# Kernel tuning notes

Hardware: AMD Instinct MI355X
Metric: run time of the kernel (lower is better)

## Reference

```python
import jax, jax.numpy as jnp
import numpy as np

N = 50000      # nodes
E = 800000     # edges (avg degree 16)
D_IN = 128
D_H = 256
NUM_LAYERS = 5


def setup_inputs() -> dict:
    key = jax.random.key(0)
    ks = jax.random.split(key, 12)
    s_in = 1.0 / np.sqrt(D_IN)
    s_h = 1.0 / np.sqrt(D_H)
    x = jax.random.normal(ks[0], (N, D_IN), jnp.float32)
    edge_index = jax.random.randint(ks[1], (2, E), 0, N, jnp.int32)
    eps_all = jnp.zeros((NUM_LAYERS,), jnp.float32)
    # torch Linear layout: weight [out, in], y = x @ W.T + b; scaled for stability
    w0_l0 = jax.random.normal(ks[2], (D_H, D_IN), jnp.float32) * s_in
    b0_l0 = jax.random.normal(ks[3], (D_H,), jnp.float32) * 0.01
    w1_l0 = jax.random.normal(ks[4], (D_H, D_H), jnp.float32) * s_h
    b1_l0 = jax.random.normal(ks[5], (D_H,), jnp.float32) * 0.01
    w0_rest = jax.random.normal(ks[6], (4, D_H, D_H), jnp.float32) * s_h
    b0_rest = jax.random.normal(ks[7], (4, D_H), jnp.float32) * 0.01
    w1_rest = jax.random.normal(ks[8], (4, D_H, D_H), jnp.float32) * s_h
    b1_rest = jax.random.normal(ks[9], (4, D_H), jnp.float32) * 0.01
    return {"x": x, "edge_index": edge_index, "eps_all": eps_all,
            "w0_l0": w0_l0, "b0_l0": b0_l0, "w1_l0": w1_l0, "b1_l0": b1_l0,
            "w0_rest": w0_rest, "b0_rest": b0_rest, "w1_rest": w1_rest, "b1_rest": b1_rest}


def _gin_layer(x, src, dst, eps, w0, b0, w1, b1):
    # gather source-node features along edges, scatter-sum into destination nodes
    aggr = jax.ops.segment_sum(x[src], dst, num_segments=N)  # [N, d]
    h = (1.0 + eps) * x + aggr
    h = jax.nn.relu(h @ w0.T + b0)   # dropout p=0.0 -> identity
    h = h @ w1.T + b1
    return jax.nn.relu(h)            # inter-layer ReLU from the trace


def reference(x, edge_index, eps_all, w0_l0, b0_l0, w1_l0, b1_l0,
              w0_rest, b0_rest, w1_rest, b1_rest):
    src = edge_index[0]  # edge_index_j (messages come from row 0)
    dst = edge_index[1]  # edge_index_i (aggregated at row 1)
    h = _gin_layer(x, src, dst, eps_all[0], w0_l0, b0_l0, w1_l0, b1_l0)
    for i in range(4):  # layers 1..4, identical shapes
        h = _gin_layer(h, src, dst, eps_all[i + 1],
                       w0_rest[i], b0_rest[i], w1_rest[i], b1_rest[i])
    return h  # [N, D_H]
```

## Files before the change

kernel.cpp:

```cpp
#include <hip/hip_runtime.h>
#include <hip/hip_bf16.h>
#include <stdint.h>

#define D_IN 128
#define D_H 256
#define NLAYERS 5

typedef __bf16 bf16x8 __attribute__((ext_vector_type(8)));
typedef float f32x4 __attribute__((ext_vector_type(4)));
typedef unsigned short u16x8 __attribute__((ext_vector_type(8)));

#define MID_STRIDE 260

__device__ inline unsigned short bfbits(float f) {
  __hip_bfloat16 h = __float2bfloat16(f);
  unsigned short s;
  __builtin_memcpy(&s, &h, 2);
  return s;
}

__device__ inline unsigned packbf(float lo, float hi) {
  return (unsigned)bfbits(lo) | ((unsigned)bfbits(hi) << 16);
}

__device__ inline void addbf2(float& a, float& b, unsigned u) {
  a += __uint_as_float(u << 16);
  b += __uint_as_float(u & 0xffff0000u);
}

__device__ inline void addbf2s(float& a, float& b, unsigned u, float s) {
  a += s * __uint_as_float(u << 16);
  b += s * __uint_as_float(u & 0xffff0000u);
}

__global__ void conv_inputs(const float* __restrict__ x, const float* __restrict__ a,
                            const float* __restrict__ b, const float* __restrict__ c,
                            const float* __restrict__ d,
                            __hip_bfloat16* __restrict__ xb,
                            __hip_bfloat16* __restrict__ wb, int nx) {
  int gid = blockIdx.x * blockDim.x + threadIdx.x;
  if (gid < nx) {
    xb[gid] = __float2bfloat16(x[gid]);
    return;
  }
  gid -= nx;
  if (gid >= 622592) return;
  float v;
  if (gid < 32768) v = a[gid];
  else if (gid < 98304) v = b[gid - 32768];
  else if (gid < 360448) v = c[gid - 98304];
  else v = d[gid - 360448];
  wb[gid] = __float2bfloat16(v);
}

__global__ void zero_ints(int* __restrict__ p, int n) {
  int i = blockIdx.x * blockDim.x + threadIdx.x;
  if (i < n) p[i] = 0;
}

#define CSR_CHUNKS 128

__global__ __launch_bounds__(256) void hist_kernel(const int* __restrict__ ei, int E,
                                                   int* __restrict__ deg, int N) {
  const int r = blockIdx.x & 7;
  const int chunk = blockIdx.x >> 3;
  const int rsize = (N + 7) >> 3;
  const int lo = r * rsize;
  const int hi = (lo + rsize < N) ? lo + rsize : N;
  const int stride = CSR_CHUNKS * 256;
  for (int e = chunk * 256 + threadIdx.x; e < E; e += stride) {
    int d = ei[E + e];
    if (d >= lo && d < hi) atomicAdd(&deg[d], 1);
  }
}

__global__ __launch_bounds__(256) void fill_kernel(const int* __restrict__ ei, int E,
                                                   const int* __restrict__ row_start,
                                                   int* __restrict__ cursor,
                                                   int* __restrict__ csr, int N) {
  const int r = blockIdx.x & 7;
  const int chunk = blockIdx.x >> 3;
  const int rsize = (N + 7) >> 3;
  const int lo = r * rsize;
  const int hi = (lo + rsize < N) ? lo + rsize : N;
  const int stride = CSR_CHUNKS * 256;
  for (int e = chunk * 256 + threadIdx.x; e < E; e += stride) {
    int d = ei[E + e];
    if (d >= lo && d < hi) {
      int p = atomicAdd(&cursor[d], 1);
      csr[row_start[d] + p] = ei[e];
    }
  }
}

__global__ __launch_bounds__(256) void block_sums(const int* __restrict__ deg,
                                                  int* __restrict__ bsum, int N) {
  int t = threadIdx.x;
  int idx = blockIdx.x * 1024 + t * 4;
  int4 v = {0, 0, 0, 0};
  if (idx + 3 < N) v = *reinterpret_cast<const int4*>(deg + idx);
  else {
    if (idx + 0 < N) v.x = deg[idx + 0];
    if (idx + 1 < N) v.y = deg[idx + 1];
    if (idx + 2 < N) v.z = deg[idx + 2];
    if (idx + 3 < N) v.w = deg[idx + 3];
  }
  int s = v.x + v.y + v.z + v.w;
#pragma unroll
  for (int off = 32; off > 0; off >>= 1) s += __shfl_down(s, off);
  __shared__ int ws[4];
  int lane = t & 63, w = t >> 6;
  if (lane == 0) ws[w] = s;
  __syncthreads();
  if (t == 0) bsum[blockIdx.x] = ws[0] + ws[1] + ws[2] + ws[3];
}

__global__ void scan_bsums(int* __restrict__ bsum, int nb) {
  int t = threadIdx.x;
  int orig = (t < nb) ? bsum[t] : 0;
  int v = orig;
#pragma unroll
  for (int off = 1; off < 64; off <<= 1) {
    int u = __shfl_up(v, off);
    if (t >= off) v += u;
  }
  if (t < nb) bsum[t] = v - orig;
}

__global__ __launch_bounds__(256) void scan_apply(const int* __restrict__ deg,
                                                  const int* __restrict__ bsum_ex,
                                                  int* __restrict__ row_start, int N) {
  int t = threadIdx.x;
  int idx = blockIdx.x * 1024 + t * 4;
  int4 v = {0, 0, 0, 0};
  if (idx + 3 < N) v = *reinterpret_cast<const int4*>(deg + idx);
  else {
    if (idx + 0 < N) v.x = deg[idx + 0];
    if (idx + 1 < N) v.y = deg[idx + 1];
    if (idx + 2 < N) v.z = deg[idx + 2];
    if (idx + 3 < N) v.w = deg[idx + 3];
  }
  int s = v.x + v.y + v.z + v.w;
  int lane = t & 63, w = t >> 6;
  int sc = s;
#pragma unroll
  for (int off = 1; off < 64; off <<= 1) {
    int u = __shfl_up(sc, off);
    if (lane >= off) sc += u;
  }
  __shared__ int woff[4];
  if (lane == 63) woff[w] = sc;
  __syncthreads();
  int boff = bsum_ex[blockIdx.x];
#pragma unroll
  for (int i = 0; i < 4; ++i)
    if (i < w) boff += woff[i];
  int ex = boff + sc - s;
  if (idx + 3 < N) {
    int4 o;
    o.x = ex;
    o.y = ex + v.x;
    o.z = ex + v.x + v.y;
    o.w = ex + v.x + v.y + v.z;
    *reinterpret_cast<int4*>(row_start + idx) = o;
  } else {
    if (idx + 0 < N) row_start[idx + 0] = ex;
    if (idx + 1 < N) row_start[idx + 1] = ex + v.x;
    if (idx + 2 < N) row_start[idx + 2] = ex + v.x + v.y;
    if (idx + 3 < N) row_start[idx + 3] = ex + v.x + v.y + v.z;
  }
}

template <int D>
__global__ __launch_bounds__(256) void aggregate(const unsigned short* __restrict__ hb,
                                                 const int* __restrict__ csr,
                                                 const int* __restrict__ row_start,
                                                 const int* __restrict__ deg,
                                                 const float* __restrict__ eps_all,
                                                 int layer,
                                                 unsigned short* __restrict__ pre,
                                                 int N) {
  constexpr int PL = D / 32;
  const int half = threadIdx.x >> 5;
  const int lane = threadIdx.x & 31;
  const int node = blockIdx.x * 8 + half;
  if (node >= N) return;

  const int start = row_start[node];
  const int cnt = deg[node];
  const float epsv = 1.0f + eps_all[layer];

  float acc[PL];
#pragma unroll
  for (int j = 0; j < PL; ++j) acc[j] = 0.0f;

  if (D == 256) {
    uint4 su = *reinterpret_cast<const uint4*>(hb + (size_t)node * D + lane * 8);
    for (int base = 0; base < cnt; base += 32) {
      int m = cnt - base;
      if (m > 32) m = 32;
      int idx = (lane < m) ? csr[start + base + lane] : 0;
      int i = 0;
      for (; i + 8 <= m; i += 8) {
        uint4 q[8];
#pragma unroll
        for (int r = 0; r < 8; ++r) {
          int s = __shfl(idx, i + r, 32);
          q[r] = *reinterpret_cast<const uint4*>(hb + (size_t)s * D + lane * 8);
        }
#pragma unroll
        for (int r = 0; r < 8; ++r) {
          addbf2(acc[0], acc[1], q[r].x);
          addbf2(acc[2], acc[3], q[r].y);
          addbf2(acc[4], acc[5], q[r].z);
          addbf2(acc[6], acc[7], q[r].w);
        }
      }
      for (; i + 4 <= m; i += 4) {
        uint4 q[4];
#pragma unroll
        for (int r = 0; r < 4; ++r) {
          int s = __shfl(idx, i + r, 32);
          q[r] = *reinterpret_cast<const uint4*>(hb + (size_t)s * D + lane * 8);
        }
#pragma unroll
        for (int r = 0; r < 4; ++r) {
          addbf2(acc[0], acc[1], q[r].x);
          addbf2(acc[2], acc[3], q[r].y);
          addbf2(acc[4], acc[5], q[r].z);
          addbf2(acc[6], acc[7], q[r].w);
        }
      }
      for (; i < m; ++i) {
        int s = __shfl(idx, i, 32);
        uint4 q = *reinterpret_cast<const uint4*>(hb + (size_t)s * D + lane * 8);
        addbf2(acc[0], acc[1], q.x);
        addbf2(acc[2], acc[3], q.y);
        addbf2(acc[4], acc[5], q.z);
        addbf2(acc[6], acc[7], q.w);
      }
    }
    addbf2s(acc[0], acc[1], su.x, epsv);
    addbf2s(acc[2], acc[3], su.y, epsv);
    addbf2s(acc[4], acc[5], su.z, epsv);
    addbf2s(acc[6], acc[7], su.w, epsv);
    uint4 o;
    o.x = packbf(acc[0], acc[1]);
    o.y = packbf(acc[2], acc[3]);
    o.z = packbf(acc[4], acc[5]);
    o.w = packbf(acc[6], acc[7]);
    *reinterpret_cast<uint4*>(pre + (size_t)node * D + lane * 8) = o;
  } else {
    uint2 su = *reinterpret_cast<const uint2*>(hb + (size_t)node * D + lane * 4);
    for (int base = 0; base < cnt; base += 32) {
      int m = cnt - base;
      if (m > 32) m = 32;
      int idx = (lane < m) ? csr[start + base + lane] : 0;
      int i = 0;
      for (; i + 8 <= m; i += 8) {
        uint2 q[8];
#pragma unroll
        for (int r = 0; r < 8; ++r) {
          int s = __shfl(idx, i + r, 32);
          q[r] = *reinterpret_cast<const uint2*>(hb + (size_t)s * D + lane * 4);
        }
#pragma unroll
        for (int r = 0; r < 8; ++r) {
          addbf2(acc[0], acc[1], q[r].x);
          addbf2(acc[2], acc[3], q[r].y);
        }
      }
      for (; i + 4 <= m; i += 4) {
        uint2 q[4];
#pragma unroll
        for (int r = 0; r < 4; ++r) {
          int s = __shfl(idx, i + r, 32);
          q[r] = *reinterpret_cast<const uint2*>(hb + (size_t)s * D + lane * 4);
        }
#pragma unroll
        for (int r = 0; r < 4; ++r) {
          addbf2(acc[0], acc[1], q[r].x);
          addbf2(acc[2], acc[3], q[r].y);
        }
      }
      for (; i < m; ++i) {
        int s = __shfl(idx, i, 32);
        uint2 q = *reinterpret_cast<const uint2*>(hb + (size_t)s * D + lane * 4);
        addbf2(acc[0], acc[1], q.x);
        addbf2(acc[2], acc[3], q.y);
      }
    }
    addbf2s(acc[0], acc[1], su.x, epsv);
    addbf2s(acc[2], acc[3], su.y, epsv);
    uint2 o;
    o.x = packbf(acc[0], acc[1]);
    o.y = packbf(acc[2], acc[3]);
    *reinterpret_cast<uint2*>(pre + (size_t)node * D + lane * 4) = o;
  }
}

template <int K0, bool OUT_BF16>
__global__ __launch_bounds__(512, 2) void mlp_fused(
    const unsigned short* __restrict__ Ap, const __hip_bfloat16* __restrict__ W0p,
    const float* __restrict__ b0, const __hip_bfloat16* __restrict__ W1p,
    const float* __restrict__ b1, void* __restrict__ Outp, int Nrows) {
  __shared__ unsigned short midb[2][32 * MID_STRIDE];

  constexpr int NK0 = K0 / 32;
  constexpr int NK1 = D_H / 32;
  const int tid = threadIdx.x;
  const int wid = tid >> 6;
  const bool prod = (wid < 4);
  const int cg = wid & 3;
  const int lane = tid & 63;
  const int l15 = lane & 15;
  const int kg = lane >> 4;
  const int col0 = cg * 64;
  const int nch = (Nrows + 31) >> 5;

  bf16x8 wfr[NK1][4];
  float bv[4];
  if (prod) {
    const unsigned short* Ws = (const unsigned short*)W0p;
#pragma unroll
    for (int ct = 0; ct < 4; ++ct) {
      const unsigned short* wrow = Ws + (size_t)(col0 + ct * 16 + l15) * K0 + kg * 8;
#pragma unroll
      for (int kk = 0; kk < NK0; ++kk)
        wfr[kk][ct] = *reinterpret_cast<const bf16x8*>(wrow + kk * 32);
      bv[ct] = b0[col0 + ct * 16 + l15];
    }
  } else {
    const unsigned short* Ws = (const unsigned short*)W1p;
#pragma unroll
    for (int ct = 0; ct < 4; ++ct) {
      const unsigned short* wrow = Ws + (size_t)(col0 + ct * 16 + l15) * D_H + kg * 8;
#pragma unroll
      for (int kk = 0; kk < NK1; ++kk)
        wfr[kk][ct] = *reinterpret_cast<const bf16x8*>(wrow + kk * 32);
      bv[ct] = b1[col0 + ct * 16 + l15];
    }
  }

  auto produce = [&](int c, unsigned short* buf) {
    const int r0 = c << 5;
    bf16x8 afr[NK0][2];
#pragma unroll
    for (int rt = 0; rt < 2; ++rt) {
      int row = r0 + rt * 16 + l15;
      if (row > Nrows - 1) row = Nrows - 1;
      const unsigned short* ar = Ap + (size_t)row * K0 + kg * 8;
#pragma unroll
      for (int kk = 0; kk < NK0; ++kk)
        afr[kk][rt] = *reinterpret_cast<const bf16x8*>(ar + kk * 32);
    }
    f32x4 acc[2][4];
#pragma unroll
    for (int rt = 0; rt < 2; ++rt)
#pragma unroll
      for (int ct = 0; ct < 4; ++ct) acc[rt][ct] = 0.0f;
#pragma unroll
    for (int kk = 0; kk < NK0; ++kk)
#pragma unroll
      for (int rt = 0; rt < 2; ++rt)
#pragma unroll
        for (int ct = 0; ct < 4; ++ct)
          acc[rt][ct] = __builtin_amdgcn_mfma_f32_16x16x32_bf16(
              afr[kk][rt], wfr[kk][ct], acc[rt][ct], 0, 0, 0);
#pragma unroll
    for (int ct = 0; ct < 4; ++ct) {
      int col = col0 + ct * 16 + l15;
#pragma unroll
      for (int rt = 0; rt < 2; ++rt)
#pragma unroll
        for (int i = 0; i < 4; ++i) {
          int row_l = rt * 16 + kg * 4 + i;
          buf[row_l * MID_STRIDE + col] = bfbits(fmaxf(acc[rt][ct][i] + bv[ct], 0.0f));
        }
    }
  };

  auto consume = [&](int c, const unsigned short* buf) {
    const int r0 = c << 5;
    f32x4 acc[2][4];
#pragma unroll
    for (int rt = 0; rt < 2; ++rt)
#pragma unroll
      for (int ct = 0; ct < 4; ++ct) acc[rt][ct] = 0.0f;
#pragma unroll
    for (int kk = 0; kk < NK1; ++kk) {
      bf16x8 mfr[2];
#pragma unroll
      for (int rt = 0; rt < 2; ++rt)
        mfr[rt] = *reinterpret_cast<const bf16x8*>(
            buf + (rt * 16 + l15) * MID_STRIDE + kk * 32 + kg * 8);
#pragma unroll
      for (int rt = 0; rt < 2; ++rt)
#pragma unroll
        for (int ct = 0; ct < 4; ++ct)
          acc[rt][ct] = __builtin_amdgcn_mfma_f32_16x16x32_bf16(
              mfr[rt], wfr[kk][ct], acc[rt][ct], 0, 0, 0);
    }
#pragma unroll
    for (int ct = 0; ct < 4; ++ct) {
      int col = col0 + ct * 16 + l15;
#pragma unroll
      for (int rt = 0; rt < 2; ++rt)
#pragma unroll
        for (int i = 0; i < 4; ++i) {
          int row = r0 + rt * 16 + kg * 4 + i;
          if (row < Nrows) {
            float v = fmaxf(acc[rt][ct][i] + bv[ct], 0.0f);
            if (OUT_BF16)
              ((__hip_bfloat16*)Outp)[(size_t)row * D_H + col] = __float2bfloat16(v);
            else
              ((float*)Outp)[(size_t)row * D_H + col] = v;
          }
        }
    }
  };

  int c_pr = blockIdx.x;
  int c_co = blockIdx.x;
  int pb = 0;
  if (prod && c_pr < nch) produce(c_pr, midb[0]);
  __syncthreads();
  c_pr += gridDim.x;
  while (c_co < nch) {
    if (prod) {
      if (c_pr < nch) produce(c_pr, midb[pb ^ 1]);
    } else {
      consume(c_co, midb[pb]);
    }
    __syncthreads();
    pb ^= 1;
    c_pr += gridDim.x;
    c_co += gridDim.x;
  }
}

extern "C" void kernel_launch(void* const* d_in, const int* in_sizes, int n_in,
                              void* d_out, int out_size, void* d_ws, size_t ws_size,
                              hipStream_t stream) {
  const float* x = (const float*)d_in[0];
  const int* ei = (const int*)d_in[1];
  const float* eps_all = (const float*)d_in[2];
  const float* w0_l0 = (const float*)d_in[3];
  const float* b0_l0 = (const float*)d_in[4];
  const float* w1_l0 = (const float*)d_in[5];
  const float* b1_l0 = (const float*)d_in[6];
  const float* w0_rest = (const float*)d_in[7];
  const float* b0_rest = (const float*)d_in[8];
  const float* w1_rest = (const float*)d_in[9];
  const float* b1_rest = (const float*)d_in[10];

  const int N = in_sizes[0] / D_IN;
  const int E = in_sizes[1] / 2;
  const int NX = N * D_IN;

  char* ws = (char*)d_ws;
  const size_t node_bf = (size_t)N * D_H * sizeof(unsigned short);
  unsigned short* h = (unsigned short*)ws;
  unsigned short* pre = (unsigned short*)(ws + node_bf);
  unsigned short* xb = (unsigned short*)(ws + 2 * node_bf);
  char* p = ws + 2 * node_bf + (size_t)NX * sizeof(unsigned short);
  __hip_bfloat16* wbf = (__hip_bfloat16*)p;
  p += 622592 * sizeof(__hip_bfloat16);
  int* deg = (int*)p;
  int* cursor = deg + N;
  int* row_start = cursor + N;
  int* bsum = row_start + N;
  int* csr = bsum + 64;

  __hip_bfloat16* w0_l0_bf = wbf;
  __hip_bfloat16* w1_l0_bf = wbf + 32768;
  __hip_bfloat16* w0_rest_bf = wbf + 98304;
  __hip_bfloat16* w1_rest_bf = w0_rest_bf + 262144;

  conv_inputs<<<(NX + 622592 + 255) / 256, 256, 0, stream>>>(
      x, w0_l0, w1_l0, w0_rest, w1_rest, (__hip_bfloat16*)xb, wbf, NX);

  const int nb = (N + 1023) / 1024;
  zero_ints<<<(2 * N + 255) / 256, 256, 0, stream>>>(deg, 2 * N);
  hist_kernel<<<8 * CSR_CHUNKS, 256, 0, stream>>>(ei, E, deg, N);
  block_sums<<<nb, 256, 0, stream>>>(deg, bsum, N);
  scan_bsums<<<1, 64, 0, stream>>>(bsum, nb);
  scan_apply<<<nb, 256, 0, stream>>>(deg, bsum, row_start, N);
  fill_kernel<<<8 * CSR_CHUNKS, 256, 0, stream>>>(ei, E, row_start, cursor, csr, N);

  const int mlpGrid = 256;
  const int aggBlocks = (N + 7) / 8;

  for (int layer = 0; layer < NLAYERS; ++layer) {
    const __hip_bfloat16* w0 =
        (layer == 0) ? w0_l0_bf : w0_rest_bf + (size_t)(layer - 1) * 65536;
    const float* b0 = (layer == 0) ? b0_l0 : b0_rest + (size_t)(layer - 1) * 256;
    const __hip_bfloat16* w1 =
        (layer == 0) ? w1_l0_bf : w1_rest_bf + (size_t)(layer - 1) * 65536;
    const float* b1 = (layer == 0) ? b1_l0 : b1_rest + (size_t)(layer - 1) * 256;

    if (layer == 0) {
      aggregate<D_IN><<<aggBlocks, 256, 0, stream>>>(xb, csr, row_start, deg,
                                                     eps_all, layer, pre, N);
      mlp_fused<D_IN, true><<<mlpGrid, 512, 0, stream>>>(pre, w0, b0, w1, b1, h, N);
    } else {
      aggregate<D_H><<<aggBlocks, 256, 0, stream>>>(h, csr, row_start, deg,
                                                    eps_all, layer, pre, N);
      if (layer == NLAYERS - 1)
        mlp_fused<D_H, false><<<mlpGrid, 512, 0, stream>>>(pre, w0, b0, w1, b1,
                                                           d_out, N);
      else
        mlp_fused<D_H, true><<<mlpGrid, 512, 0, stream>>>(pre, w0, b0, w1, b1, h, N);
    }
  }
}
```

Baseline: 509.1 us.

## Double MLP chunk rows, fold block-sum scan into apply, use memset

The fused MLP kernel now handles 64-row chunks per pipeline stage, run as two 32-row sub-tiles, so there are half as many chunks and barriers, at the cost of twice the shared memory per buffer. The separate single-block scan of block sums is removed: each scan_apply block reduces the preceding block sums itself. The zeroing kernel is replaced by hipMemsetAsync. Together these cut kernel launches and synchronisation, but the larger LDS footprint may lower occupancy.

```diff
diff --git a/kernel.cpp b/kernel.cpp
--- a/kernel.cpp
+++ b/kernel.cpp
@@ -51,11 +51,6 @@
   else if (gid < 360448) v = c[gid - 98304];
   else v = d[gid - 360448];
   wb[gid] = __float2bfloat16(v);
-}
-
-__global__ void zero_ints(int* __restrict__ p, int n) {
-  int i = blockIdx.x * blockDim.x + threadIdx.x;
-  if (i < n) p[i] = 0;
 }
 
 #define CSR_CHUNKS 128
@@ -115,22 +110,18 @@
   if (t == 0) bsum[blockIdx.x] = ws[0] + ws[1] + ws[2] + ws[3];
 }
 
-__global__ void scan_bsums(int* __restrict__ bsum, int nb) {
+__global__ __launch_bounds__(256) void scan_apply(const int* __restrict__ deg,
+                                                  const int* __restrict__ bsum,
+                                                  int* __restrict__ row_start, int N) {
+  __shared__ int woff[4];
+  __shared__ int boff_sh;
   int t = threadIdx.x;
-  int orig = (t < nb) ? bsum[t] : 0;
-  int v = orig;
-#pragma unroll
-  for (int off = 1; off < 64; off <<= 1) {
-    int u = __shfl_up(v, off);
-    if (t >= off) v += u;
-  }
-  if (t < nb) bsum[t] = v - orig;
-}
-
-__global__ __launch_bounds__(256) void scan_apply(const int* __restrict__ deg,
-                                                  const int* __restrict__ bsum_ex,
-                                                  int* __restrict__ row_start, int N) {
-  int t = threadIdx.x;
+  if (t < 64) {
+    int v = (t < blockIdx.x) ? bsum[t] : 0;
+#pragma unroll
+    for (int off = 32; off > 0; off >>= 1) v += __shfl_down(v, off);
+    if (t == 0) boff_sh = v;
+  }
   int idx = blockIdx.x * 1024 + t * 4;
   int4 v = {0, 0, 0, 0};
   if (idx + 3 < N) v = *reinterpret_cast<const int4*>(deg + idx);
@@ -148,10 +139,9 @@
     int u = __shfl_up(sc, off);
     if (lane >= off) sc += u;
   }
-  __shared__ int woff[4];
   if (lane == 63) woff[w] = sc;
   __syncthreads();
-  int boff = bsum_ex[blockIdx.x];
+  int boff = boff_sh;
 #pragma unroll
   for (int i = 0; i < 4; ++i)
     if (i < w) boff += woff[i];
@@ -304,7 +294,7 @@
     const unsigned short* __restrict__ Ap, const __hip_bfloat16* __restrict__ W0p,
     const float* __restrict__ b0, const __hip_bfloat16* __restrict__ W1p,
     const float* __restrict__ b1, void* __restrict__ Outp, int Nrows) {
-  __shared__ unsigned short midb[2][32 * MID_STRIDE];
+  __shared__ unsigned short midb[2][64 * MID_STRIDE];
 
   constexpr int NK0 = K0 / 32;
   constexpr int NK1 = D_H / 32;
@@ -316,7 +306,7 @@
   const int l15 = lane & 15;
   const int kg = lane >> 4;
   const int col0 = cg * 64;
-  const int nch = (Nrows + 31) >> 5;
+  const int nch = (Nrows + 63) >> 6;
 
   bf16x8 wfr[NK1][4];
   float bv[4];
@@ -343,80 +333,87 @@
   }
 
   auto produce = [&](int c, unsigned short* buf) {
-    const int r0 = c << 5;
-    bf16x8 afr[NK0][2];
-#pragma unroll
-    for (int rt = 0; rt < 2; ++rt) {
-      int row = r0 + rt * 16 + l15;
-      if (row > Nrows - 1) row = Nrows - 1;
-      const unsigned short* ar = Ap + (size_t)row * K0 + kg * 8;
+#pragma unroll
+    for (int sub = 0; sub < 2; ++sub) {
+      const int r0 = (c << 6) + sub * 32;
+      bf16x8 afr[NK0][2];
+#pragma unroll
+      for (int rt = 0; rt < 2; ++rt) {
+        int row = r0 + rt * 16 + l15;
+        if (row > Nrows - 1) row = Nrows - 1;
+        const unsigned short* ar = Ap + (size_t)row * K0 + kg * 8;
+#pragma unroll
+        for (int kk = 0; kk < NK0; ++kk)
+          afr[kk][rt] = *reinterpret_cast<const bf16x8*>(ar + kk * 32);
+      }
+      f32x4 acc[2][4];
+#pragma unroll
+      for (int rt = 0; rt < 2; ++rt)
+#pragma unroll
+        for (int ct = 0; ct < 4; ++ct) acc[rt][ct] = 0.0f;
 #pragma unroll
       for (int kk = 0; kk < NK0; ++kk)
-        afr[kk][rt] = *reinterpret_cast<const bf16x8*>(ar + kk * 32);
-    }
-    f32x4 acc[2][4];
-#pragma unroll
-    for (int rt = 0; rt < 2; ++rt)
-#pragma unroll
-      for (int ct = 0; ct < 4; ++ct) acc[rt][ct] = 0.0f;
-#pragma unroll
-    for (int kk = 0; kk < NK0; ++kk)
+#pragma unroll
+        for (int rt = 0; rt < 2; ++rt)
+#pragma unroll
+          for (int ct = 0; ct < 4; ++ct)
+            acc[rt][ct] = __builtin_amdgcn_mfma_f32_16x16x32_bf16(
+                afr[kk][rt], wfr[kk][ct], acc[rt][ct], 0, 0, 0);
+#pragma unroll
+      for (int ct = 0; ct < 4; ++ct) {
+        int col = col0 + ct * 16 + l15;
+#pragma unroll
+        for (int rt = 0; rt < 2; ++rt)
+#pragma unroll
+          for (int i = 0; i < 4; ++i) {
+            int row_l = sub * 32 + rt * 16 + kg * 4 + i;
+            buf[row_l * MID_STRIDE + col] =
+                bfbits(fmaxf(acc[rt][ct][i] + bv[ct], 0.0f));
+          }
+      }
+    }
+  };
+
+  auto consume = [&](int c, const unsigned short* buf) {
+#pragma unroll
+    for (int sub = 0; sub < 2; ++sub) {
+      const int r0 = (c << 6) + sub * 32;
+      f32x4 acc[2][4];
 #pragma unroll
       for (int rt = 0; rt < 2; ++rt)
 #pragma unroll
-        for (int ct = 0; ct < 4; ++ct)
-          acc[rt][ct] = __builtin_amdgcn_mfma_f32_16x16x32_bf16(
-              afr[kk][rt], wfr[kk][ct], acc[rt][ct], 0, 0, 0);
-#pragma unroll
-    for (int ct = 0; ct < 4; ++ct) {
-      int col = col0 + ct * 16 + l15;
-#pragma unroll
-      for (int rt = 0; rt < 2; ++rt)
-#pragma unroll
-        for (int i = 0; i < 4; ++i) {
-          int row_l = rt * 16 + kg * 4 + i;
-          buf[row_l * MID_STRIDE + col] = bfbits(fmaxf(acc[rt][ct][i] + bv[ct], 0.0f));
-        }
-    }
-  };
-
-  auto consume = [&](int c, const unsigned short* buf) {
-    const int r0 = c << 5;
-    f32x4 acc[2][4];
-#pragma unroll
-    for (int rt = 0; rt < 2; ++rt)
-#pragma unroll
-      for (int ct = 0; ct < 4; ++ct) acc[rt][ct] = 0.0f;
-#pragma unroll
-    for (int kk = 0; kk < NK1; ++kk) {
-      bf16x8 mfr[2];
-#pragma unroll
-      for (int rt = 0; rt < 2; ++rt)
-        mfr[rt] = *reinterpret_cast<const bf16x8*>(
-            buf + (rt * 16 + l15) * MID_STRIDE + kk * 32 + kg * 8);
-#pragma unroll
-      for (int rt = 0; rt < 2; ++rt)
-#pragma unroll
-        for (int ct = 0; ct < 4; ++ct)
-          acc[rt][ct] = __builtin_amdgcn_mfma_f32_16x16x32_bf16(
-              mfr[rt], wfr[kk][ct], acc[rt][ct], 0, 0, 0);
-    }
-#pragma unroll
-    for (int ct = 0; ct < 4; ++ct) {
-      int col = col0 + ct * 16 + l15;
-#pragma unroll
-      for (int rt = 0; rt < 2; ++rt)
-#pragma unroll
-        for (int i = 0; i < 4; ++i) {
-          int row = r0 + rt * 16 + kg * 4 + i;
-          if (row < Nrows) {
-            float v = fmaxf(acc[rt][ct][i] + bv[ct], 0.0f);
-            if (OUT_BF16)
-              ((__hip_bfloat16*)Outp)[(size_t)row * D_H + col] = __float2bfloat16(v);
-            else
-              ((float*)Outp)[(size_t)row * D_H + col] = v;
+        for (int ct = 0; ct < 4; ++ct) acc[rt][ct] = 0.0f;
+#pragma unroll
+      for (int kk = 0; kk < NK1; ++kk) {
+        bf16x8 mfr[2];
+#pragma unroll
+        for (int rt = 0; rt < 2; ++rt)
+          mfr[rt] = *reinterpret_cast<const bf16x8*>(
+              buf + (sub * 32 + rt * 16 + l15) * MID_STRIDE + kk * 32 + kg * 8);
+#pragma unroll
+        for (int rt = 0; rt < 2; ++rt)
+#pragma unroll
+          for (int ct = 0; ct < 4; ++ct)
+            acc[rt][ct] = __builtin_amdgcn_mfma_f32_16x16x32_bf16(
+                mfr[rt], wfr[kk][ct], acc[rt][ct], 0, 0, 0);
+      }
+#pragma unroll
+      for (int ct = 0; ct < 4; ++ct) {
+        int col = col0 + ct * 16 + l15;
+#pragma unroll
+        for (int rt = 0; rt < 2; ++rt)
+#pragma unroll
+          for (int i = 0; i < 4; ++i) {
+            int row = r0 + rt * 16 + kg * 4 + i;
+            if (row < Nrows) {
+              float v = fmaxf(acc[rt][ct][i] + bv[ct], 0.0f);
+              if (OUT_BF16)
+                ((__hip_bfloat16*)Outp)[(size_t)row * D_H + col] = __float2bfloat16(v);
+              else
+                ((float*)Outp)[(size_t)row * D_H + col] = v;
+            }
           }
-        }
+      }
     }
   };
 
@@ -481,10 +478,9 @@
       x, w0_l0, w1_l0, w0_rest, w1_rest, (__hip_bfloat16*)xb, wbf, NX);
 
   const int nb = (N + 1023) / 1024;
-  zero_ints<<<(2 * N + 255) / 256, 256, 0, stream>>>(deg, 2 * N);
+  hipMemsetAsync(deg, 0, (size_t)2 * N * sizeof(int), stream);
   hist_kernel<<<8 * CSR_CHUNKS, 256, 0, stream>>>(ei, E, deg, N);
   block_sums<<<nb, 256, 0, stream>>>(deg, bsum, N);
-  scan_bsums<<<1, 64, 0, stream>>>(bsum, nb);
   scan_apply<<<nb, 256, 0, stream>>>(deg, bsum, row_start, N);
   fill_kernel<<<8 * CSR_CHUNKS, 256, 0, stream>>>(ei, E, row_start, cursor, csr, N);
 
```

After: 546.6 us. +7.4%, slower.
